# Kernel optimization log

Measured on AMD Instinct MI355X. Metric: run time of the kernel, lower is better.

The kernel has to match this reference:

```python
import jax, jax.numpy as jnp
import numpy as np

GROUP = 32  # values per quantization group (per-group scale)

def setup_inputs() -> dict:
    key = jax.random.key(0)
    k1, k2, k3, k4 = jax.random.split(key, 4)
    B, S, IN, OUT = 4, 2048, 4096, 4096
    x = jax.random.normal(k1, (B, S, IN), dtype=jnp.float32)
    # packed 4-bit weights: each int32 byte-value in [0,256) holds two nibbles
    w_packed = jax.random.randint(k2, (OUT, IN // 2), 0, 256, dtype=jnp.int32)
    scales = jax.random.uniform(k3, (OUT, IN // GROUP), dtype=jnp.float32) * 0.02 + 0.001
    bias = jax.random.normal(k4, (OUT,), dtype=jnp.float32)
    return {"x": x, "w_packed": w_packed, "scales": scales, "bias": bias}

def _dequantize(w_packed, scales):
    # w_packed: [OUT, IN//2] int32 bytes, scales: [OUT, IN//GROUP]
    OUT = w_packed.shape[0]
    low = w_packed & 0xF
    high = (w_packed >> 4) & 0xF
    q = jnp.stack([low, high], axis=-1).reshape(OUT, -1)  # [OUT, IN]
    qf = q.astype(jnp.float32) - 8.0  # signed 4-bit centered at 8
    qg = qf.reshape(OUT, scales.shape[1], GROUP)
    w = qg * scales[:, :, None]
    return w.reshape(OUT, -1)  # [OUT, IN]

def reference(x, w_packed, scales, bias):
    # dequantize weights then F.linear: y = x @ W^T + b
    W = _dequantize(w_packed, scales)  # [OUT, IN]
    y = jnp.einsum('bsi,oi->bso', x, W) + bias
    return y
```

## Files before the change

### kernel.cpp

```cpp
#include <hip/hip_runtime.h>
#include <stdint.h>

#define M_TOT 8192
#define K_TOT 4096
#define N_TOT 4096
#define GROUPQ 32

#define BM 256
#define BN 256
#define BK 64
#define NT (K_TOT / BK)

typedef __bf16 bf16x8 __attribute__((ext_vector_type(8)));
typedef float f32x4 __attribute__((ext_vector_type(4)));
typedef unsigned short u16;
typedef unsigned short u16x8 __attribute__((ext_vector_type(8)));

template <int V> struct IC { static constexpr int value = V; };

__device__ __forceinline__ u16 f2bf_rne(float f) {
  union { float f; uint32_t u; } v; v.f = f;
  uint32_t u = v.u;
  uint32_t r = (u + 0x7FFFu + ((u >> 16) & 1u)) >> 16;
  return (u16)r;
}

__global__ void cvt_x_kernel(const float* __restrict__ x, u16* __restrict__ xb, int n8) {
  int stride = gridDim.x * blockDim.x;
  for (int i = blockIdx.x * blockDim.x + threadIdx.x; i < n8; i += stride) {
    const float4* p = (const float4*)(x + (size_t)i * 8);
    float4 a = p[0];
    float4 b = p[1];
    u16x8 o;
    o[0] = f2bf_rne(a.x); o[1] = f2bf_rne(a.y); o[2] = f2bf_rne(a.z); o[3] = f2bf_rne(a.w);
    o[4] = f2bf_rne(b.x); o[5] = f2bf_rne(b.y); o[6] = f2bf_rne(b.z); o[7] = f2bf_rne(b.w);
    *(u16x8*)(xb + (size_t)i * 8) = o;
  }
}

__global__ void dequant_w_kernel(const int* __restrict__ wp, const float* __restrict__ sc,
                                 u16* __restrict__ wb) {
  const int KH = K_TOT / 2;
  const int total = N_TOT * KH / 8;
  int stride = gridDim.x * blockDim.x;
  for (int t = blockIdx.x * blockDim.x + threadIdx.x; t < total; t += stride) {
    int base = t * 8;
    int o = base >> 11;
    int ci = base & 2047;
    int e0 = ci * 2;
    float scale = sc[o * (K_TOT / GROUPQ) + (e0 >> 5)];
    int4 p0 = *(const int4*)(wp + base);
    int4 p1 = *(const int4*)(wp + base + 4);
    int v[8] = {p0.x, p0.y, p0.z, p0.w, p1.x, p1.y, p1.z, p1.w};
    u16x8 oA, oB;
#pragma unroll
    for (int j = 0; j < 8; ++j) {
      float lo = (float)((v[j] & 0xF) - 8) * scale;
      float hi = (float)(((v[j] >> 4) & 0xF) - 8) * scale;
      u16 lob = f2bf_rne(lo), hib = f2bf_rne(hi);
      if (j < 4) { oA[2 * j] = lob; oA[2 * j + 1] = hib; }
      else       { oB[2 * (j - 4)] = lob; oB[2 * (j - 4) + 1] = hib; }
    }
    u16* dst = wb + (size_t)o * K_TOT + e0;
    *(u16x8*)dst = oA;
    *(u16x8*)(dst + 8) = oB;
  }
}

__global__ __launch_bounds__(512, 2) void gemm_bf16_kernel(
    const u16* __restrict__ A, const u16* __restrict__ Bt,
    const float* __restrict__ bias, float* __restrict__ C) {
  __shared__ alignas(16) u16 sL[65536];

  const int ntn = N_TOT / BN;
  int wg = blockIdx.x, nwg = gridDim.x;
  int cpx = nwg >> 3;
  int swz = (wg & 7) * cpx + (wg >> 3);
  int bm = swz / ntn, bn = swz % ntn;

  int tid = threadIdx.x, wid = tid >> 6, lane = tid & 63;
  int wr = wid >> 2, wc = wid & 3;
  const size_t K = K_TOT;

  int rowS = tid >> 2;
  int cgS = (tid & 3) ^ ((rowS >> 1) & 3);
  const u16* pA = A + ((size_t)(bm * 256 + (rowS >> 6) * 128 + (rowS & 63))) * K + cgS * 8;
  const u16* pB = Bt + ((size_t)(bn * 256 + (rowS >> 5) * 64 + (rowS & 31))) * K + cgS * 8;
  u16* sE = &sL[0];

#define GLLDS(src, dst)                                                      \
  __builtin_amdgcn_global_load_lds(                                          \
      (const __attribute__((address_space(1))) uint32_t*)(src),              \
      (__attribute__((address_space(3))) uint32_t*)(dst), 16, 0, 0)

  auto stA = [&](int T, int mh, auto bufc) {
    constexpr int buf = decltype(bufc)::value;
    const u16* s = pA + (size_t)mh * 64 * K + (size_t)T * 64;
    GLLDS(s,      sE + ((buf * 2 + 0) * 2 + mh) * 4096 + tid * 8);
    GLLDS(s + 32, sE + ((buf * 2 + 1) * 2 + mh) * 4096 + tid * 8);
  };
  auto stB = [&](int T, int nh, auto bufc) {
    constexpr int buf = decltype(bufc)::value;
    const u16* s = pB + (size_t)nh * 32 * K + (size_t)T * 64;
    GLLDS(s,      sE + 32768 + ((buf * 2 + 0) * 2 + nh) * 4096 + tid * 8);
    GLLDS(s + 32, sE + 32768 + ((buf * 2 + 1) * 2 + nh) * 4096 + tid * 8);
  };

  int rA = wr * 64 + (lane & 15);
  int cA = ((lane >> 4) ^ ((rA >> 1) & 3)) * 8;
  int rB = wc * 32 + (lane & 15);
  int cB = ((lane >> 4) ^ ((rB >> 1) & 3)) * 8;
  const u16* rdA = sE + rA * 32 + cA;
  const u16* rdB = sE + 32768 + rB * 32 + cB;
  auto ldA = [&](auto bufc, int kk, int mh, int m3) {
    constexpr int buf = decltype(bufc)::value;
    return *(const bf16x8*)(rdA + ((buf * 2 + kk) * 2 + mh) * 4096 + m3 * 16 * 32);
  };
  auto ldB = [&](auto bufc, int kk, int nh, int n2) {
    constexpr int buf = decltype(bufc)::value;
    return *(const bf16x8*)(rdB + ((buf * 2 + kk) * 2 + nh) * 4096 + n2 * 16 * 32);
  };

  f32x4 acc[8][4] = {};
  bf16x8 a0[4][2], a1[4][2], b0[2][2], b1[2][2];

  stA(0, 0, IC<0>{}); stB(0, 0, IC<0>{}); stB(0, 1, IC<0>{}); stA(0, 1, IC<0>{});
  stA(1, 0, IC<1>{}); stB(1, 0, IC<1>{}); stB(1, 1, IC<1>{}); stA(1, 1, IC<1>{});
  asm volatile("s_waitcnt vmcnt(4)" ::: "memory");
  __builtin_amdgcn_s_barrier();

#pragma unroll
  for (int m3 = 0; m3 < 4; ++m3)
#pragma unroll
    for (int kk = 0; kk < 2; ++kk) a0[m3][kk] = ldA(IC<0>{}, kk, 0, m3);
#pragma unroll
  for (int n2 = 0; n2 < 2; ++n2)
#pragma unroll
    for (int kk = 0; kk < 2; ++kk) b0[n2][kk] = ldB(IC<0>{}, kk, 0, n2);
  asm volatile("s_waitcnt lgkmcnt(0)" ::: "memory");
  __builtin_amdgcn_s_barrier();

  auto tile_body = [&](int t, auto bufc, auto nbufc) {
    constexpr int BUFV = decltype(bufc)::value;
    (void)BUFV;
    bool st_ok = (t + 2 < NT);
    bool rd_ok = (t + 1 < NT);
    int Ts = t + 2;

#pragma unroll
    for (int n2 = 0; n2 < 2; ++n2)
#pragma unroll
      for (int kk = 0; kk < 2; ++kk) b1[n2][kk] = ldB(bufc, kk, 1, n2);
    if (st_ok) stA(Ts, 0, bufc);
    __builtin_amdgcn_s_setprio(1);
#pragma unroll
    for (int kk = 0; kk < 2; ++kk)
#pragma unroll
      for (int m3 = 0; m3 < 4; ++m3)
#pragma unroll
        for (int n2 = 0; n2 < 2; ++n2)
          acc[m3][n2] = __builtin_amdgcn_mfma_f32_16x16x32_bf16(a0[m3][kk], b0[n2][kk], acc[m3][n2], 0, 0, 0);
    __builtin_amdgcn_s_setprio(0);

#pragma unroll
    for (int m3 = 0; m3 < 4; ++m3)
#pragma unroll
      for (int kk = 0; kk < 2; ++kk) a1[m3][kk] = ldA(bufc, kk, 1, m3);
    if (st_ok) stB(Ts, 0, bufc);
    __builtin_amdgcn_s_setprio(1);
#pragma unroll
    for (int kk = 0; kk < 2; ++kk)
#pragma unroll
      for (int m3 = 0; m3 < 4; ++m3)
#pragma unroll
        for (int n2 = 0; n2 < 2; ++n2)
          acc[m3][n2 + 2] = __builtin_amdgcn_mfma_f32_16x16x32_bf16(a0[m3][kk], b1[n2][kk], acc[m3][n2 + 2], 0, 0, 0);
    __builtin_amdgcn_s_setprio(0);
    __builtin_amdgcn_s_barrier();

    if (rd_ok) {
#pragma unroll
      for (int m3 = 0; m3 < 4; ++m3)
#pragma unroll
        for (int kk = 0; kk < 2; ++kk) a0[m3][kk] = ldA(nbufc, kk, 0, m3);
    }
    if (st_ok) stB(Ts, 1, bufc);
    __builtin_amdgcn_s_setprio(1);
#pragma unroll
    for (int kk = 0; kk < 2; ++kk)
#pragma unroll
      for (int m3 = 0; m3 < 4; ++m3)
#pragma unroll
        for (int n2 = 0; n2 < 2; ++n2)
          acc[m3 + 4][n2] = __builtin_amdgcn_mfma_f32_16x16x32_bf16(a1[m3][kk], b0[n2][kk], acc[m3 + 4][n2], 0, 0, 0);
    __builtin_amdgcn_s_setprio(0);
    __builtin_amdgcn_s_barrier();

    if (rd_ok) {
#pragma unroll
      for (int n2 = 0; n2 < 2; ++n2)
#pragma unroll
        for (int kk = 0; kk < 2; ++kk) b0[n2][kk] = ldB(nbufc, kk, 0, n2);
    }
    if (st_ok) stA(Ts, 1, bufc);
    __builtin_amdgcn_s_setprio(1);
#pragma unroll
    for (int kk = 0; kk < 2; ++kk)
#pragma unroll
      for (int m3 = 0; m3 < 4; ++m3)
#pragma unroll
        for (int n2 = 0; n2 < 2; ++n2)
          acc[m3 + 4][n2 + 2] = __builtin_amdgcn_mfma_f32_16x16x32_bf16(a1[m3][kk], b1[n2][kk], acc[m3 + 4][n2 + 2], 0, 0, 0);
    __builtin_amdgcn_s_setprio(0);
    asm volatile("s_waitcnt lgkmcnt(0)" ::: "memory");
    if (t < NT - 2) { asm volatile("s_waitcnt vmcnt(4)" ::: "memory"); }
    else            { asm volatile("s_waitcnt vmcnt(0)" ::: "memory"); }
    __builtin_amdgcn_s_barrier();
  };

  for (int t = 0; t < NT; t += 2) {
    tile_body(t,     IC<0>{}, IC<1>{});
    tile_body(t + 1, IC<1>{}, IC<0>{});
  }

  asm volatile("s_waitcnt vmcnt(0)" ::: "memory");

  int col = lane & 15;
  int rb = (lane >> 4) * 4;
#pragma unroll
  for (int n = 0; n < 4; ++n) {
    int gn = bn * BN + wc * 64 + n * 16 + col;
    float bsv = bias[gn];
#pragma unroll
    for (int m = 0; m < 8; ++m) {
      int gm = bm * BM + wr * 128 + m * 16 + rb;
#pragma unroll
      for (int j = 0; j < 4; ++j)
        C[(size_t)(gm + j) * N_TOT + gn] = acc[m][n][j] + bsv;
    }
  }
#undef GLLDS
}

__global__ void fill_kernel(float* p, int n, float v) {
  int stride = gridDim.x * blockDim.x;
  for (int i = blockIdx.x * blockDim.x + threadIdx.x; i < n; i += stride) p[i] = v;
}

extern "C" void kernel_launch(void* const* d_in, const int* in_sizes, int n_in,
                              void* d_out, int out_size, void* d_ws, size_t ws_size,
                              hipStream_t stream) {
  const float* x = (const float*)d_in[0];
  const int* wp = (const int*)d_in[1];
  const float* sc = (const float*)d_in[2];
  const float* bias = (const float*)d_in[3];
  float* out = (float*)d_out;

  size_t xb_bytes = (size_t)M_TOT * K_TOT * 2;
  size_t wb_bytes = (size_t)N_TOT * K_TOT * 2;
  if (ws_size < xb_bytes + wb_bytes) {
    fill_kernel<<<2048, 256, 0, stream>>>(out, out_size, 12345.0f);
    return;
  }
  u16* xb = (u16*)d_ws;
  u16* wb = (u16*)((char*)d_ws + xb_bytes);

  cvt_x_kernel<<<2048, 256, 0, stream>>>(x, xb, M_TOT * K_TOT / 8);
  dequant_w_kernel<<<2048, 256, 0, stream>>>(wp, sc, wb);
  gemm_bf16_kernel<<<(M_TOT / BM) * (N_TOT / BN), 512, 0, stream>>>(xb, wb, bias, out);
}
```

Measured before the change: 268.7 us.

## Fuse fp32-to-bf16 conversion of activations into GEMM A-tile loading

Drops the separate x conversion kernel. The GEMM now loads fp32 activations into registers, converts them to bf16 and writes them to LDS, replacing the direct global-to-LDS loads for the A operand. The loads are software-pipelined a tile ahead, with the vmcnt waits adjusted to match. This removes a full write and re-read of the bf16 copy of x, but raises register pressure and doubles the A-side global read bytes per tile inside the GEMM.

```diff
diff --git a/kernel.cpp b/kernel.cpp
--- a/kernel.cpp
+++ b/kernel.cpp
@@ -23,19 +23,6 @@
   uint32_t u = v.u;
   uint32_t r = (u + 0x7FFFu + ((u >> 16) & 1u)) >> 16;
   return (u16)r;
-}
-
-__global__ void cvt_x_kernel(const float* __restrict__ x, u16* __restrict__ xb, int n8) {
-  int stride = gridDim.x * blockDim.x;
-  for (int i = blockIdx.x * blockDim.x + threadIdx.x; i < n8; i += stride) {
-    const float4* p = (const float4*)(x + (size_t)i * 8);
-    float4 a = p[0];
-    float4 b = p[1];
-    u16x8 o;
-    o[0] = f2bf_rne(a.x); o[1] = f2bf_rne(a.y); o[2] = f2bf_rne(a.z); o[3] = f2bf_rne(a.w);
-    o[4] = f2bf_rne(b.x); o[5] = f2bf_rne(b.y); o[6] = f2bf_rne(b.z); o[7] = f2bf_rne(b.w);
-    *(u16x8*)(xb + (size_t)i * 8) = o;
-  }
 }
 
 __global__ void dequant_w_kernel(const int* __restrict__ wp, const float* __restrict__ sc,
@@ -68,7 +55,7 @@
 }
 
 __global__ __launch_bounds__(512, 2) void gemm_bf16_kernel(
-    const u16* __restrict__ A, const u16* __restrict__ Bt,
+    const float* __restrict__ X, const u16* __restrict__ Bt,
     const float* __restrict__ bias, float* __restrict__ C) {
   __shared__ alignas(16) u16 sL[65536];
 
@@ -84,7 +71,7 @@
 
   int rowS = tid >> 2;
   int cgS = (tid & 3) ^ ((rowS >> 1) & 3);
-  const u16* pA = A + ((size_t)(bm * 256 + (rowS >> 6) * 128 + (rowS & 63))) * K + cgS * 8;
+  const float* pX = X + ((size_t)(bm * 256 + (rowS >> 6) * 128 + (rowS & 63))) * K + cgS * 8;
   const u16* pB = Bt + ((size_t)(bn * 256 + (rowS >> 5) * 64 + (rowS & 31))) * K + cgS * 8;
   u16* sE = &sL[0];
 
@@ -93,17 +80,44 @@
       (const __attribute__((address_space(1))) uint32_t*)(src),              \
       (__attribute__((address_space(3))) uint32_t*)(dst), 16, 0, 0)
 
-  auto stA = [&](int T, int mh, auto bufc) {
-    constexpr int buf = decltype(bufc)::value;
-    const u16* s = pA + (size_t)mh * 64 * K + (size_t)T * 64;
-    GLLDS(s,      sE + ((buf * 2 + 0) * 2 + mh) * 4096 + tid * 8);
-    GLLDS(s + 32, sE + ((buf * 2 + 1) * 2 + mh) * 4096 + tid * 8);
-  };
   auto stB = [&](int T, int nh, auto bufc) {
     constexpr int buf = decltype(bufc)::value;
     const u16* s = pB + (size_t)nh * 32 * K + (size_t)T * 64;
     GLLDS(s,      sE + 32768 + ((buf * 2 + 0) * 2 + nh) * 4096 + tid * 8);
     GLLDS(s + 32, sE + 32768 + ((buf * 2 + 1) * 2 + nh) * 4096 + tid * 8);
+  };
+
+  float4 fA0_0, fA0_1, fA0_2, fA0_3;
+  float4 fA1_0, fA1_1, fA1_2, fA1_3;
+  auto loadA0 = [&](int T, int mh) {
+    const float* s = pX + (size_t)mh * 64 * K + (size_t)T * 64;
+    fA0_0 = *(const float4*)(s);
+    fA0_1 = *(const float4*)(s + 4);
+    fA0_2 = *(const float4*)(s + 32);
+    fA0_3 = *(const float4*)(s + 36);
+  };
+  auto loadA1 = [&](int T, int mh) {
+    const float* s = pX + (size_t)mh * 64 * K + (size_t)T * 64;
+    fA1_0 = *(const float4*)(s);
+    fA1_1 = *(const float4*)(s + 4);
+    fA1_2 = *(const float4*)(s + 32);
+    fA1_3 = *(const float4*)(s + 36);
+  };
+  auto cvt8 = [](const float4& a, const float4& b) {
+    bf16x8 v;
+    v[0] = (__bf16)a.x; v[1] = (__bf16)a.y; v[2] = (__bf16)a.z; v[3] = (__bf16)a.w;
+    v[4] = (__bf16)b.x; v[5] = (__bf16)b.y; v[6] = (__bf16)b.z; v[7] = (__bf16)b.w;
+    return v;
+  };
+  auto wrA0 = [&](auto bufc, int mh) {
+    constexpr int buf = decltype(bufc)::value;
+    *(bf16x8*)(sE + ((buf * 2 + 0) * 2 + mh) * 4096 + tid * 8) = cvt8(fA0_0, fA0_1);
+    *(bf16x8*)(sE + ((buf * 2 + 1) * 2 + mh) * 4096 + tid * 8) = cvt8(fA0_2, fA0_3);
+  };
+  auto wrA1 = [&](auto bufc, int mh) {
+    constexpr int buf = decltype(bufc)::value;
+    *(bf16x8*)(sE + ((buf * 2 + 0) * 2 + mh) * 4096 + tid * 8) = cvt8(fA1_0, fA1_1);
+    *(bf16x8*)(sE + ((buf * 2 + 1) * 2 + mh) * 4096 + tid * 8) = cvt8(fA1_2, fA1_3);
   };
 
   int rA = wr * 64 + (lane & 15);
@@ -124,9 +138,15 @@
   f32x4 acc[8][4] = {};
   bf16x8 a0[4][2], a1[4][2], b0[2][2], b1[2][2];
 
-  stA(0, 0, IC<0>{}); stB(0, 0, IC<0>{}); stB(0, 1, IC<0>{}); stA(0, 1, IC<0>{});
-  stA(1, 0, IC<1>{}); stB(1, 0, IC<1>{}); stB(1, 1, IC<1>{}); stA(1, 1, IC<1>{});
+  stB(0, 0, IC<0>{}); stB(0, 1, IC<0>{});
+  stB(1, 0, IC<1>{}); stB(1, 1, IC<1>{});
+  loadA0(0, 0); loadA1(0, 1);
+  wrA0(IC<0>{}, 0); wrA1(IC<0>{}, 1);
+  loadA0(1, 0); loadA1(1, 1);
+  wrA0(IC<1>{}, 0); wrA1(IC<1>{}, 1);
+  loadA0(2, 0);
   asm volatile("s_waitcnt vmcnt(4)" ::: "memory");
+  asm volatile("s_waitcnt lgkmcnt(0)" ::: "memory");
   __builtin_amdgcn_s_barrier();
 
 #pragma unroll
@@ -141,8 +161,6 @@
   __builtin_amdgcn_s_barrier();
 
   auto tile_body = [&](int t, auto bufc, auto nbufc) {
-    constexpr int BUFV = decltype(bufc)::value;
-    (void)BUFV;
     bool st_ok = (t + 2 < NT);
     bool rd_ok = (t + 1 < NT);
     int Ts = t + 2;
@@ -151,7 +169,7 @@
     for (int n2 = 0; n2 < 2; ++n2)
 #pragma unroll
       for (int kk = 0; kk < 2; ++kk) b1[n2][kk] = ldB(bufc, kk, 1, n2);
-    if (st_ok) stA(Ts, 0, bufc);
+    if (st_ok) wrA0(bufc, 0);
     __builtin_amdgcn_s_setprio(1);
 #pragma unroll
     for (int kk = 0; kk < 2; ++kk)
@@ -166,7 +184,7 @@
     for (int m3 = 0; m3 < 4; ++m3)
 #pragma unroll
       for (int kk = 0; kk < 2; ++kk) a1[m3][kk] = ldA(bufc, kk, 1, m3);
-    if (st_ok) stB(Ts, 0, bufc);
+    if (st_ok) { stB(Ts, 0, bufc); loadA1(Ts, 1); }
     __builtin_amdgcn_s_setprio(1);
 #pragma unroll
     for (int kk = 0; kk < 2; ++kk)
@@ -185,6 +203,7 @@
         for (int kk = 0; kk < 2; ++kk) a0[m3][kk] = ldA(nbufc, kk, 0, m3);
     }
     if (st_ok) stB(Ts, 1, bufc);
+    if (t + 3 < NT) loadA0(t + 3, 0);
     __builtin_amdgcn_s_setprio(1);
 #pragma unroll
     for (int kk = 0; kk < 2; ++kk)
@@ -202,7 +221,7 @@
 #pragma unroll
         for (int kk = 0; kk < 2; ++kk) b0[n2][kk] = ldB(nbufc, kk, 0, n2);
     }
-    if (st_ok) stA(Ts, 1, bufc);
+    if (st_ok) wrA1(bufc, 1);
     __builtin_amdgcn_s_setprio(1);
 #pragma unroll
     for (int kk = 0; kk < 2; ++kk)
@@ -213,7 +232,7 @@
           acc[m3 + 4][n2 + 2] = __builtin_amdgcn_mfma_f32_16x16x32_bf16(a1[m3][kk], b1[n2][kk], acc[m3 + 4][n2 + 2], 0, 0, 0);
     __builtin_amdgcn_s_setprio(0);
     asm volatile("s_waitcnt lgkmcnt(0)" ::: "memory");
-    if (t < NT - 2) { asm volatile("s_waitcnt vmcnt(4)" ::: "memory"); }
+    if (t < NT - 2) { asm volatile("s_waitcnt vmcnt(10)" ::: "memory"); }
     else            { asm volatile("s_waitcnt vmcnt(0)" ::: "memory"); }
     __builtin_amdgcn_s_barrier();
   };
@@ -256,16 +275,13 @@
   const float* bias = (const float*)d_in[3];
   float* out = (float*)d_out;
 
-  size_t xb_bytes = (size_t)M_TOT * K_TOT * 2;
   size_t wb_bytes = (size_t)N_TOT * K_TOT * 2;
-  if (ws_size < xb_bytes + wb_bytes) {
+  if (ws_size < wb_bytes) {
     fill_kernel<<<2048, 256, 0, stream>>>(out, out_size, 12345.0f);
     return;
   }
-  u16* xb = (u16*)d_ws;
-  u16* wb = (u16*)((char*)d_ws + xb_bytes);
-
-  cvt_x_kernel<<<2048, 256, 0, stream>>>(x, xb, M_TOT * K_TOT / 8);
+  u16* wb = (u16*)d_ws;
+
   dequant_w_kernel<<<2048, 256, 0, stream>>>(wp, sc, wb);
-  gemm_bf16_kernel<<<(M_TOT / BM) * (N_TOT / BN), 512, 0, stream>>>(xb, wb, bias, out);
-}
+  gemm_bf16_kernel<<<(M_TOT / BM) * (N_TOT / BN), 512, 0, stream>>>(x, wb, bias, out);
+}
```

New measurement: 1.064 ms. +295.9%, slower.
